# Performance work log

Hardware: AMD Instinct MI355X
Metric: run time of the kernel (lower is better)

## Reference

```python
import jax, jax.numpy as jnp
import numpy as np

B, S, D, H, BS, L, FF, V = 2, 4096, 1024, 16, 64, 4, 4096, 50000
HD = D // H; NB = S // BS; NM = NB - 2; R = 3

def layernorm(x, g, b):
    mu = x.mean(-1, keepdims=True)
    var = ((x - mu) ** 2).mean(-1, keepdims=True)
    return (x - mu) * jax.lax.rsqrt(var + 1e-5) * g + b

def bigbird_attn(x, neg, rand_attn, Wq, bq, Wk, bk, Wv, bv, Wo, bo):
    heads = lambda t: t.reshape(B, S, H, HD).transpose(0, 2, 1, 3)
    q, k, v = heads(x @ Wq + bq), heads(x @ Wk + bk), heads(x @ Wv + bv)
    scale = np.float32(1.0 / np.sqrt(HD))
    qb = q.reshape(B, H, NB, BS, HD); kb = k.reshape(B, H, NB, BS, HD); vb = v.reshape(B, H, NB, BS, HD)
    negb = neg.reshape(B, NB, BS)
    # global query blocks (first & last) attend densely to all keys
    qg = jnp.concatenate([qb[:, :, 0], qb[:, :, -1]], axis=2)  # [B,H,2*BS,HD]
    sg = jnp.einsum('bhqd,bhkd->bhqk', qg, k) * scale + neg[:, None, None, :]
    ctx_g = jnp.einsum('bhqk,bhkd->bhqd', jax.nn.softmax(sg, -1), v)
    # middle query blocks: sliding window(3) + global(2) + random(R) key blocks
    win_k = jnp.stack([kb[:, :, i:i + NM] for i in range(3)], axis=3)  # [B,H,NM,3,BS,HD]
    win_v = jnp.stack([vb[:, :, i:i + NM] for i in range(3)], axis=3)
    gidx = jnp.array([0, NB - 1])
    g_k = jnp.broadcast_to(kb[:, :, gidx][:, :, None], (B, H, NM, 2, BS, HD))
    g_v = jnp.broadcast_to(vb[:, :, gidx][:, :, None], (B, H, NM, 2, BS, HD))
    hix = jnp.arange(H)[:, None, None]
    r_k = kb[:, hix, rand_attn]  # [B,H,NM,R,BS,HD]
    r_v = vb[:, hix, rand_attn]
    K = 3 + 2 + R
    keys = jnp.concatenate([win_k, g_k, r_k], axis=3).reshape(B, H, NM, K * BS, HD)
    vals = jnp.concatenate([win_v, g_v, r_v], axis=3).reshape(B, H, NM, K * BS, HD)
    win_m = jnp.stack([negb[:, i:i + NM] for i in range(3)], axis=2)  # [B,NM,3,BS]
    g_m = jnp.broadcast_to(negb[:, gidx][:, None], (B, NM, 2, BS))
    m_wg = jnp.concatenate([win_m, g_m], axis=2).reshape(B, 1, NM, 5 * BS)
    r_m = negb[:, rand_attn].reshape(B, H, NM, R * BS)
    m_all = jnp.concatenate([jnp.broadcast_to(m_wg, (B, H, NM, 5 * BS)), r_m], axis=-1)
    sm = jnp.einsum('bhnqd,bhnkd->bhnqk', qb[:, :, 1:-1], keys) * scale + m_all[:, :, :, None, :]
    ctx_m = jnp.einsum('bhnqk,bhnkd->bhnqd', jax.nn.softmax(sm, -1), vals)
    ctx = jnp.concatenate([ctx_g[:, :, None, :BS], ctx_m, ctx_g[:, :, None, BS:]], axis=2)
    out = ctx.reshape(B, H, S, HD).transpose(0, 2, 1, 3).reshape(B, S, D)
    return out @ Wo + bo

def reference(input_ids, attention_mask, rand_attn, emb, Wq, bq, Wk, bk, Wv, bv, Wo, bo, ln1_g, ln1_b, W1, b1, W2, b2, ln2_g, ln2_b, lnf_g, lnf_b, projW, projb):
    x = emb[input_ids]
    neg = (1.0 - attention_mask.astype(jnp.float32)) * (-1e9)
    for l in range(L):  # pre-norm transformer encoder layers
        x = x + bigbird_attn(layernorm(x, ln1_g[l], ln1_b[l]), neg, rand_attn,
                             Wq[l], bq[l], Wk[l], bk[l], Wv[l], bv[l], Wo[l], bo[l])
        h = layernorm(x, ln2_g[l], ln2_b[l])
        x = x + (jax.nn.gelu(h @ W1[l] + b1[l]) @ W2[l] + b2[l])
    x = layernorm(x, lnf_g, lnf_b)
    feats = x.mean(axis=1)  # pooled output (mean over tokens)
    feats = feats / jnp.maximum(jnp.linalg.norm(feats, axis=-1, keepdims=True), 1e-12)
    return feats @ projW + projb

def setup_inputs():
    key = jax.random.key(0)
    ks = jax.random.split(key, 16)
    init = lambda k, shp: (0.02 * jax.random.normal(k, shp)).astype(jnp.float32)
    return {
        'input_ids': jax.random.randint(ks[0], (B, S), 0, V),
        'attention_mask': jnp.ones((B, S), dtype=jnp.int32),
        'rand_attn': jax.random.randint(ks[1], (H, NM, R), 1, NB - 1),
        'emb': init(ks[2], (V, D)),
        'Wq': init(ks[3], (L, D, D)), 'bq': jnp.zeros((L, D), jnp.float32),
        'Wk': init(ks[4], (L, D, D)), 'bk': jnp.zeros((L, D), jnp.float32),
        'Wv': init(ks[5], (L, D, D)), 'bv': jnp.zeros((L, D), jnp.float32),
        'Wo': init(ks[6], (L, D, D)), 'bo': jnp.zeros((L, D), jnp.float32),
        'ln1_g': jnp.ones((L, D), jnp.float32), 'ln1_b': jnp.zeros((L, D), jnp.float32),
        'W1': init(ks[7], (L, D, FF)), 'b1': jnp.zeros((L, FF), jnp.float32),
        'W2': init(ks[8], (L, FF, D)), 'b2': jnp.zeros((L, D), jnp.float32),
        'ln2_g': jnp.ones((L, D), jnp.float32), 'ln2_b': jnp.zeros((L, D), jnp.float32),
        'lnf_g': jnp.ones((D,), jnp.float32), 'lnf_b': jnp.zeros((D,), jnp.float32),
        'projW': init(ks[9], (D, 512)), 'projb': jnp.zeros((512,), jnp.float32),
    }
```

## Files before the change

kernel.cpp:

```cpp
#include <hip/hip_runtime.h>
#include <hip/hip_bf16.h>
#include <cstdint>
#include <cstddef>

#define BATCH 2
#define SEQ   4096
#define DIM   1024
#define NHEAD 16
#define HDIM  64
#define NBLK  64
#define NMID  62
#define NRAND 3
#define NLAYER 4
#define FFDIM 4096
#define ROWS  (BATCH*SEQ)
#define KSPL  8
#define QKVLD (3*DIM)
#define WLAYER (12*1024*1024)

using f32x4 = __attribute__((ext_vector_type(4))) float;
using s16x8 = __attribute__((ext_vector_type(8))) short;
using s16x4 = __attribute__((ext_vector_type(4))) short;

__device__ inline float bf2f(short s) {
    unsigned u = ((unsigned)(unsigned short)s) << 16;
    union { unsigned u; float f; } cv; cv.u = u; return cv.f;
}
__device__ inline short f2bf(float f) {
    union { float f; unsigned u; } cv; cv.f = f;
    unsigned u = cv.u;
    unsigned r = (u + 0x7fffu + ((u >> 16) & 1u)) >> 16;
    return (short)r;
}
__device__ inline float gelu_f(float x) {
    float u = 0.7978845608028654f * (x + 0.044715f * x * x * x);
    float a = fabsf(u);
    float th = 1.f - 2.f / (1.f + __expf(2.f * a));
    th = copysignf(th, u);
    return 0.5f * x * (1.f + th);
}

__device__ inline void gload16(const short* g, short* l) {
    __builtin_amdgcn_global_load_lds(
        (const __attribute__((address_space(1))) void*)g,
        (__attribute__((address_space(3))) void*)l,
        16, 0, 0);
}

__global__ __launch_bounds__(256) void embed_kernel(
    const int* __restrict__ ids, const float* __restrict__ emb, float* __restrict__ x)
{
    int row = blockIdx.x;
    int id  = ids[row];
    ((float4*)x)[(size_t)row * 256 + threadIdx.x] =
        ((const float4*)emb)[(size_t)id * 256 + threadIdx.x];
}

__global__ __launch_bounds__(256) void neg_kernel(
    const int* __restrict__ mask, float* __restrict__ neg)
{
    int i = blockIdx.x * 256 + threadIdx.x;
    if (i < ROWS) neg[i] = (1.f - (float)mask[i]) * -1e9f;
}

__global__ __launch_bounds__(256) void biaspack_kernel(
    const float* __restrict__ bq, const float* __restrict__ bk,
    const float* __restrict__ bv, float* __restrict__ b3)
{
    int i = blockIdx.x * 256 + threadIdx.x;
    float v = (i < DIM) ? bq[i] : (i < 2 * DIM) ? bk[i - DIM] : bv[i - 2 * DIM];
    b3[i] = v;
}

template<int OUTBF>
__global__ __launch_bounds__(256) void ln_kernel(
    const float* __restrict__ x, const float* __restrict__ g,
    const float* __restrict__ bia, void* __restrict__ out)
{
    __shared__ float s1[4], s2[4];
    int row = blockIdx.x, t = threadIdx.x;
    const float* xr = x + (size_t)row * DIM;
    float4 v = ((const float4*)xr)[t];
    float s = v.x + v.y + v.z + v.w;
    #pragma unroll
    for (int o = 32; o > 0; o >>= 1) s += __shfl_xor(s, o, 64);
    if ((t & 63) == 0) s1[t >> 6] = s;
    __syncthreads();
    float mu = (s1[0] + s1[1] + s1[2] + s1[3]) * (1.f / DIM);
    float dx = v.x - mu, dy = v.y - mu, dz = v.z - mu, dw = v.w - mu;
    float q = dx*dx + dy*dy + dz*dz + dw*dw;
    #pragma unroll
    for (int o = 32; o > 0; o >>= 1) q += __shfl_xor(q, o, 64);
    if ((t & 63) == 0) s2[t >> 6] = q;
    __syncthreads();
    float var = (s2[0] + s2[1] + s2[2] + s2[3]) * (1.f / DIM);
    float rs  = rsqrtf(var + 1e-5f);
    float4 gg = ((const float4*)g)[t];
    float4 bb = ((const float4*)bia)[t];
    float o0 = dx * rs * gg.x + bb.x;
    float o1 = dy * rs * gg.y + bb.y;
    float o2 = dz * rs * gg.z + bb.z;
    float o3 = dw * rs * gg.w + bb.w;
    if (OUTBF) {
        s16x4 ov = { f2bf(o0), f2bf(o1), f2bf(o2), f2bf(o3) };
        ((s16x4*)out)[(size_t)row * (DIM/4) + t] = ov;
    } else {
        float4 ov = { o0, o1, o2, o3 };
        ((float4*)out)[(size_t)row * (DIM/4) + t] = ov;
    }
}

__global__ __launch_bounds__(256) void wconv_kernel(
    const float* __restrict__ W, short* __restrict__ Wt, int K, int N)
{
    __shared__ float tile[32][33];
    int k0 = blockIdx.x * 32, n0 = blockIdx.y * 32;
    int t = threadIdx.x;
    int r = t >> 3, c = (t & 7) * 4;
    float4 v = *(const float4*)(W + (size_t)(k0 + r) * N + n0 + c);
    tile[r][c+0] = v.x; tile[r][c+1] = v.y; tile[r][c+2] = v.z; tile[r][c+3] = v.w;
    __syncthreads();
    s16x4 ov;
    #pragma unroll
    for (int jj = 0; jj < 4; ++jj) ov[jj] = f2bf(tile[c + jj][r]);
    *(s16x4*)(Wt + (size_t)(n0 + r) * K + k0 + c) = ov;
}

__global__ __launch_bounds__(256) void vtrans_kernel(
    const short* __restrict__ qkv, short* __restrict__ vT)
{
    __shared__ short tile[64][66];
    const int sb = blockIdx.x, h = blockIdx.y, b = blockIdx.z;
    const int t = threadIdx.x;
    {
        int row = t >> 2, c0 = (t & 3) * 16;
        const short* src = qkv + 2 * DIM + (size_t)(b * SEQ + sb * 64 + row) * QKVLD + h * HDIM + c0;
        s16x8 a0 = ((const s16x8*)src)[0];
        s16x8 a1 = ((const s16x8*)src)[1];
        #pragma unroll
        for (int i = 0; i < 8; ++i) { tile[row][c0 + i] = a0[i]; tile[row][c0 + 8 + i] = a1[i]; }
    }
    __syncthreads();
    {
        int d = t >> 2, k0 = (t & 3) * 16;
        s16x8 o0, o1;
        #pragma unroll
        for (int i = 0; i < 8; ++i) { o0[i] = tile[k0 + i][d]; o1[i] = tile[k0 + 8 + i][d]; }
        short* dst = vT + (size_t)((b * NHEAD + h) * HDIM + d) * SEQ + sb * 64 + k0;
        ((s16x8*)dst)[0] = o0;
        ((s16x8*)dst)[1] = o1;
    }
}

template<int EPI>
__global__ __launch_bounds__(512) void gemm256_kernel(
    const short* __restrict__ A, const short* __restrict__ Bt,
    const float* __restrict__ bias, const float* __restrict__ resid,
    void* __restrict__ Cout, int M, int N, int K, int klen)
{
    __shared__ short As[2][256 * 64];
    __shared__ short Bs[2][256 * 64];
    const int t = threadIdx.x;
    const int m0 = blockIdx.x * 256, n0 = blockIdx.y * 256;
    const int lane = t & 63, wave = t >> 6;
    const int wm = wave >> 2, wn = wave & 3;
    const int l15 = lane & 15;
    const int lrow = lane >> 3;
    const int lksw = ((lane & 7) ^ lrow) * 8;
    const int ga = wn;
    const int hb = wn >> 1, gb = wm * 2 + (wn & 1);

    f32x4 acc[8][4];
    #pragma unroll
    for (int m = 0; m < 8; ++m)
        #pragma unroll
        for (int n = 0; n < 4; ++n)
            acc[m][n] = f32x4{0.f, 0.f, 0.f, 0.f};

    auto STAGE_A = [&](int side, int kt) {
        #pragma unroll
        for (int c = 0; c < 4; ++c) {
            int row = wm * 128 + c * 32 + ga * 8 + lrow;
            gload16(A + (size_t)(m0 + row) * K + kt + lksw,
                    &As[side][wm * 8192 + c * 2048 + ga * 512]);
        }
    };
    auto STAGE_B = [&](int side, int kt) {
        #pragma unroll
        for (int c = 0; c < 4; ++c) {
            int row = hb * 128 + c * 32 + gb * 8 + lrow;
            gload16(Bt + (size_t)(n0 + row) * K + kt + lksw,
                    &Bs[side][hb * 8192 + c * 2048 + gb * 512]);
        }
    };
    auto RD_A = [&](const short* buf, int mf, int kk) -> s16x8 {
        int r = wm * 128 + mf * 16 + l15;
        int cb = kk * 64 + (lane >> 4) * 16;
        return *(const s16x8*)((const char*)buf + r * 128 + (cb ^ ((r & 7) << 4)));
    };
    auto RD_B = [&](const short* buf, int nf, int kk) -> s16x8 {
        int r = wn * 64 + nf * 16 + l15;
        int cb = kk * 64 + (lane >> 4) * 16;
        return *(const s16x8*)((const char*)buf + r * 128 + (cb ^ ((r & 7) << 4)));
    };

    const int k0 = blockIdx.z * klen, kend = k0 + klen;
    STAGE_A(0, k0);
    STAGE_B(0, k0);
    asm volatile("s_waitcnt vmcnt(0)" ::: "memory");
    __syncthreads();

    int cur = 0;
    for (int kt = k0; kt < kend; kt += 64) {
        const short* Ac = As[cur];
        const short* Bc = Bs[cur];
        const bool nxt = (kt + 64 < kend);
        s16x8 af[4][2], bf[2][2], bf2[2][2];

        #pragma unroll
        for (int mf = 0; mf < 4; ++mf) { af[mf][0] = RD_A(Ac, mf, 0); af[mf][1] = RD_A(Ac, mf, 1); }
        #pragma unroll
        for (int nf = 0; nf < 2; ++nf) { bf[nf][0] = RD_B(Bc, nf, 0); bf[nf][1] = RD_B(Bc, nf, 1); }
        if (nxt) STAGE_A(cur ^ 1, kt + 64);
        __builtin_amdgcn_s_barrier();
        __builtin_amdgcn_s_setprio(1);
        #pragma unroll
        for (int kk = 0; kk < 2; ++kk)
            #pragma unroll
            for (int mf = 0; mf < 4; ++mf)
                #pragma unroll
                for (int nf = 0; nf < 2; ++nf)
                    acc[mf][nf] = __builtin_amdgcn_mfma_f32_16x16x32_bf16(af[mf][kk], bf[nf][kk], acc[mf][nf], 0, 0, 0);
        __builtin_amdgcn_s_setprio(0);
        __builtin_amdgcn_s_barrier();

        #pragma unroll
        for (int nf = 0; nf < 2; ++nf) { bf2[nf][0] = RD_B(Bc, 2 + nf, 0); bf2[nf][1] = RD_B(Bc, 2 + nf, 1); }
        if (nxt) STAGE_B(cur ^ 1, kt + 64);
        __builtin_amdgcn_s_barrier();
        __builtin_amdgcn_s_setprio(1);
        #pragma unroll
        for (int kk = 0; kk < 2; ++kk)
            #pragma unroll
            for (int mf = 0; mf < 4; ++mf)
                #pragma unroll
                for (int nf = 0; nf < 2; ++nf)
                    acc[mf][2 + nf] = __builtin_amdgcn_mfma_f32_16x16x32_bf16(af[mf][kk], bf2[nf][kk], acc[mf][2 + nf], 0, 0, 0);
        __builtin_amdgcn_s_setprio(0);
        __builtin_amdgcn_s_barrier();

        #pragma unroll
        for (int mf = 0; mf < 4; ++mf) { af[mf][0] = RD_A(Ac, 4 + mf, 0); af[mf][1] = RD_A(Ac, 4 + mf, 1); }
        __builtin_amdgcn_s_barrier();
        __builtin_amdgcn_s_setprio(1);
        #pragma unroll
        for (int kk = 0; kk < 2; ++kk)
            #pragma unroll
            for (int mf = 0; mf < 4; ++mf)
                #pragma unroll
                for (int nf = 0; nf < 2; ++nf)
                    acc[4 + mf][nf] = __builtin_amdgcn_mfma_f32_16x16x32_bf16(af[mf][kk], bf[nf][kk], acc[4 + mf][nf], 0, 0, 0);
        __builtin_amdgcn_s_setprio(0);
        __builtin_amdgcn_s_barrier();

        asm volatile("s_waitcnt vmcnt(0)" ::: "memory");
        __builtin_amdgcn_s_barrier();
        __builtin_amdgcn_s_setprio(1);
        #pragma unroll
        for (int kk = 0; kk < 2; ++kk)
            #pragma unroll
            for (int mf = 0; mf < 4; ++mf)
                #pragma unroll
                for (int nf = 0; nf < 2; ++nf)
                    acc[4 + mf][2 + nf] = __builtin_amdgcn_mfma_f32_16x16x32_bf16(af[mf][kk], bf2[nf][kk], acc[4 + mf][2 + nf], 0, 0, 0);
        __builtin_amdgcn_s_setprio(0);
        __builtin_amdgcn_s_barrier();

        cur ^= 1;
    }

    const int rbase = m0 + wm * 128 + ((lane >> 4) << 2);
    const int cbase = n0 + wn * 64 + l15;
    #pragma unroll
    for (int m = 0; m < 8; ++m) {
        #pragma unroll
        for (int n = 0; n < 4; ++n) {
            #pragma unroll
            for (int j = 0; j < 4; ++j) {
                int row = rbase + m * 16 + j;
                int col = cbase + n * 16;
                size_t idx = (size_t)row * N + col;
                float val = acc[m][n][j];
                if (EPI == 3) {
                    ((float*)Cout)[(size_t)blockIdx.z * ((size_t)M * N) + idx] = val;
                } else {
                    val += bias[col];
                    if (EPI == 1) val = gelu_f(val);
                    ((short*)Cout)[idx] = f2bf(val);
                }
            }
        }
    }
    (void)resid;
}

template<int EPI>
__global__ __launch_bounds__(256) void gemm_kernel(
    const short* __restrict__ A, const short* __restrict__ Bt,
    const float* __restrict__ bias, const float* __restrict__ resid,
    void* __restrict__ Cout, int M, int N, int K, int klen)
{
    __shared__ short As[128 * 64];
    __shared__ short Bs[128 * 64];
    const int t = threadIdx.x;
    const int m0 = blockIdx.x * 128, n0 = blockIdx.y * 128;
    const int lane = t & 63, wave = t >> 6;
    const int wr = (wave >> 1) * 64, wc = (wave & 1) * 64;
    const int lrow = lane >> 3;
    const int lksw = ((lane & 7) ^ lrow) * 8;

    f32x4 acc[4][4];
    #pragma unroll
    for (int m = 0; m < 4; ++m)
        #pragma unroll
        for (int n = 0; n < 4; ++n)
            acc[m][n] = f32x4{0.f, 0.f, 0.f, 0.f};

    const int k0 = blockIdx.z * klen;
    for (int kt = k0; kt < k0 + klen; kt += 64) {
        #pragma unroll
        for (int c = 0; c < 4; ++c) {
            int chunk = wave * 4 + c;
            int row = chunk * 8 + lrow;
            gload16(A  + (size_t)(m0 + row) * K + kt + lksw, As + chunk * 512);
            gload16(Bt + (size_t)(n0 + row) * K + kt + lksw, Bs + chunk * 512);
        }
        asm volatile("s_waitcnt vmcnt(0)" ::: "memory");
        __syncthreads();
        #pragma unroll
        for (int kk = 0; kk < 2; ++kk) {
            s16x8 af[4], bfr[4];
            int cb = kk * 64 + (lane >> 4) * 16;
            #pragma unroll
            for (int i = 0; i < 4; ++i) {
                int rA = wr + i * 16 + (lane & 15);
                af[i]  = *(const s16x8*)((const char*)As + rA * 128 + (cb ^ ((rA & 7) << 4)));
                int rB = wc + i * 16 + (lane & 15);
                bfr[i] = *(const s16x8*)((const char*)Bs + rB * 128 + (cb ^ ((rB & 7) << 4)));
            }
            #pragma unroll
            for (int m = 0; m < 4; ++m)
                #pragma unroll
                for (int n = 0; n < 4; ++n)
                    acc[m][n] = __builtin_amdgcn_mfma_f32_16x16x32_bf16(
                        af[m], bfr[n], acc[m][n], 0, 0, 0);
        }
        __syncthreads();
    }

    const int rbase = m0 + wr + ((lane >> 4) << 2);
    const int cbase = n0 + wc + (lane & 15);
    #pragma unroll
    for (int m = 0; m < 4; ++m) {
        #pragma unroll
        for (int n = 0; n < 4; ++n) {
            #pragma unroll
            for (int j = 0; j < 4; ++j) {
                int row = rbase + m * 16 + j;
                int col = cbase + n * 16;
                size_t idx = (size_t)row * N + col;
                float val = acc[m][n][j] + bias[col];
                if (EPI == 1) val = gelu_f(val);
                if (EPI == 2) ((float*)Cout)[idx] = val + resid[idx];
                else          ((short*)Cout)[idx] = f2bf(val);
            }
        }
    }
}

__global__ __launch_bounds__(256) void kred_kernel(
    const float* __restrict__ part, const float* __restrict__ bias, float* __restrict__ x)
{
    const size_t MN = (size_t)ROWS * DIM;
    size_t idx = (size_t)blockIdx.x * DIM + threadIdx.x * 4;
    float4 p0 = *(const float4*)(part + idx);
    float4 p1 = *(const float4*)(part + MN + idx);
    float4 bb = *(const float4*)(bias + threadIdx.x * 4);
    float4 xv = *(const float4*)(x + idx);
    float4 o = { xv.x + p0.x + p1.x + bb.x,
                 xv.y + p0.y + p1.y + bb.y,
                 xv.z + p0.z + p1.z + bb.z,
                 xv.w + p0.w + p1.w + bb.w };
    *(float4*)(x + idx) = o;
}

__device__ inline void attn_tile_mfma(
    const short* __restrict__ kglob, const short* __restrict__ vtglob,
    const float* __restrict__ negp, int kld,
    short* Ks, short* Vs, float* kmask,
    const s16x8* qfrag, f32x4* o, float& mr, float& lsum)
{
    const int t = threadIdx.x;
    const int lane = t & 63;
    const int q15 = lane & 15, g = lane >> 4;
    const int sw = (lane & 7) << 4;

    {
        int row = t >> 2, c0 = (t & 3) * 16;
        int rsw = (row & 7) << 4;
        const short* ksrc = kglob + (size_t)row * kld + c0;
        s16x8 a0 = ((const s16x8*)ksrc)[0];
        s16x8 a1 = ((const s16x8*)ksrc)[1];
        char* kdst = (char*)Ks + row * 128;
        *(s16x8*)(kdst + ((c0 * 2)      ^ rsw)) = a0;
        *(s16x8*)(kdst + ((c0 * 2 + 16) ^ rsw)) = a1;
        const short* vsrc = vtglob + (size_t)row * SEQ + c0;
        s16x8 b0 = ((const s16x8*)vsrc)[0];
        s16x8 b1 = ((const s16x8*)vsrc)[1];
        char* vdst = (char*)Vs + row * 128;
        *(s16x8*)(vdst + ((c0 * 2)      ^ rsw)) = b0;
        *(s16x8*)(vdst + ((c0 * 2 + 16) ^ rsw)) = b1;
        if (t < 16) ((float4*)kmask)[t] = ((const float4*)negp)[t];
    }
    __syncthreads();

    f32x4 s[4];
    #pragma unroll
    for (int f = 0; f < 4; ++f) s[f] = f32x4{0.f, 0.f, 0.f, 0.f};
    #pragma unroll
    for (int ch = 0; ch < 2; ++ch) {
        #pragma unroll
        for (int f = 0; f < 4; ++f) {
            s16x8 kf = *(const s16x8*)((const char*)Ks + (16 * f + q15) * 128 + ((ch * 64 + g * 16) ^ sw));
            s[f] = __builtin_amdgcn_mfma_f32_16x16x32_bf16(kf, qfrag[ch], s[f], 0, 0, 0);
        }
    }

    float p[4][4];
    float mt = -1e30f;
    #pragma unroll
    for (int f = 0; f < 4; ++f) {
        float4 km = ((const float4*)kmask)[f * 4 + g];
        #pragma unroll
        for (int j = 0; j < 4; ++j) {
            float val = s[f][j] * 0.125f + ((const float*)&km)[j];
            p[f][j] = val;
            mt = fmaxf(mt, val);
        }
    }
    mt = fmaxf(mt, __shfl_xor(mt, 16, 64));
    mt = fmaxf(mt, __shfl_xor(mt, 32, 64));
    float mn = fmaxf(mr, mt);
    float psum = 0.f;
    #pragma unroll
    for (int f = 0; f < 4; ++f)
        #pragma unroll
        for (int j = 0; j < 4; ++j) {
            float e = __expf(p[f][j] - mn);
            p[f][j] = e;
            psum += e;
        }
    psum += __shfl_xor(psum, 16, 64);
    psum += __shfl_xor(psum, 32, 64);
    float fc = __expf(mr - mn);
    mr = mn;
    lsum = lsum * fc + psum;
    #pragma unroll
    for (int dt = 0; dt < 4; ++dt)
        #pragma unroll
        for (int j = 0; j < 4; ++j) o[dt][j] *= fc;

    unsigned pk[4][2];
    #pragma unroll
    for (int f = 0; f < 4; ++f)
        #pragma unroll
        for (int pp = 0; pp < 2; ++pp)
            pk[f][pp] = ((unsigned)(unsigned short)f2bf(p[f][2 * pp + 1]) << 16)
                      |  (unsigned)(unsigned short)f2bf(p[f][2 * pp]);

    const int bsel = (lane >> 4) & 1, asel = (lane >> 5) & 1;
    #pragma unroll
    for (int c = 0; c < 2; ++c) {
        union { s16x8 v; int u[4]; } pb;
        #pragma unroll
        for (int w = 0; w < 4; ++w) {
            int src = q15 + 16 * (2 * bsel + (w >> 1));
            int lo = __shfl((int)pk[2 * c][w & 1], src, 64);
            int hi = __shfl((int)pk[2 * c + 1][w & 1], src, 64);
            pb.u[w] = asel ? hi : lo;
        }
        #pragma unroll
        for (int dt = 0; dt < 4; ++dt) {
            s16x8 vf = *(const s16x8*)((const char*)Vs + (16 * dt + q15) * 128 + ((c * 64 + g * 16) ^ sw));
            o[dt] = __builtin_amdgcn_mfma_f32_16x16x32_bf16(vf, pb.v, o[dt], 0, 0, 0);
        }
    }
    __syncthreads();
}

__device__ inline void stage_q64_swz(const short* __restrict__ qglob, int qld, short* Qs)
{
    int t = threadIdx.x;
    int row = t >> 2, c0 = (t & 3) * 16;
    int rsw = (row & 7) << 4;
    const short* src = qglob + (size_t)row * qld + c0;
    s16x8 a0 = ((const s16x8*)src)[0];
    s16x8 a1 = ((const s16x8*)src)[1];
    char* dst = (char*)Qs + row * 128;
    *(s16x8*)(dst + ((c0 * 2)      ^ rsw)) = a0;
    *(s16x8*)(dst + ((c0 * 2 + 16) ^ rsw)) = a1;
}

__global__ __launch_bounds__(256) void attn_middle_mfma(
    const short* __restrict__ qkv, const short* __restrict__ vT,
    const float* __restrict__ neg, const int* __restrict__ rand_attn, short* __restrict__ ctx)
{
    __shared__ short Qs[64 * 64];
    __shared__ short Ks[64 * 64];
    __shared__ short Vs[64 * 64];
    __shared__ float kmask[64];

    const int j = blockIdx.x, h = blockIdx.y, b = blockIdx.z;
    const int n = j + 1;
    const int t = threadIdx.x;
    const int lane = t & 63, wave = t >> 6;
    const int q15 = lane & 15, g = lane >> 4;
    const int sw = (lane & 7) << 4;

    stage_q64_swz(qkv + (size_t)(b * SEQ + n * 64) * QKVLD + h * HDIM, QKVLD, Qs);
    __syncthreads();

    s16x8 qfrag[2];
    {
        int qrow = wave * 16 + q15;
        #pragma unroll
        for (int ch = 0; ch < 2; ++ch)
            qfrag[ch] = *(const s16x8*)((const char*)Qs + qrow * 128 + ((ch * 64 + g * 16) ^ sw));
    }

    int kbl[8];
    kbl[0] = n - 1; kbl[1] = n; kbl[2] = n + 1; kbl[3] = 0; kbl[4] = NBLK - 1;
    {
        const int* ra = rand_attn + ((size_t)h * NMID + j) * NRAND;
        kbl[5] = ra[0]; kbl[6] = ra[1]; kbl[7] = ra[2];
    }

    f32x4 o[4];
    #pragma unroll
    for (int dt = 0; dt < 4; ++dt) o[dt] = f32x4{0.f, 0.f, 0.f, 0.f};
    float mr = -1e30f, lsum = 0.f;

    const short* kbase  = qkv + DIM + (size_t)b * SEQ * QKVLD + h * HDIM;
    const short* vtbase = vT + (size_t)(b * NHEAD + h) * HDIM * SEQ;
    const float* negb   = neg + (size_t)b * SEQ;

    #pragma unroll 1
    for (int ib = 0; ib < 8; ++ib) {
        int kbn = kbl[ib];
        attn_tile_mfma(kbase + (size_t)kbn * 64 * QKVLD, vtbase + kbn * 64,
                       negb + kbn * 64, QKVLD, Ks, Vs, kmask, qfrag, o, mr, lsum);
    }

    float inv = 1.f / lsum;
    short* obase = ctx + (size_t)(b * SEQ + n * 64 + wave * 16 + q15) * DIM + h * HDIM;
    #pragma unroll
    for (int dt = 0; dt < 4; ++dt) {
        s16x4 ov;
        #pragma unroll
        for (int jj = 0; jj < 4; ++jj) ov[jj] = f2bf(o[dt][jj] * inv);
        *(s16x4*)(obase + dt * 16 + g * 4) = ov;
    }
}

__global__ __launch_bounds__(256) void attn_global_mfma(
    const short* __restrict__ qkv, const short* __restrict__ vT,
    const float* __restrict__ neg, float* __restrict__ part)
{
    __shared__ short Qs[64 * 64];
    __shared__ short Ks[64 * 64];
    __shared__ short Vs[64 * 64];
    __shared__ float kmask[64];

    const int qb = blockIdx.x >> 3, ks = blockIdx.x & 7;
    const int h = blockIdx.y, b = blockIdx.z;
    const int tok0 = qb ? (SEQ - 64) : 0;
    const int t = threadIdx.x;
    const int lane = t & 63, wave = t >> 6;
    const int q15 = lane & 15, g = lane >> 4;
    const int sw = (lane & 7) << 4;

    stage_q64_swz(qkv + (size_t)(b * SEQ + tok0) * QKVLD + h * HDIM, QKVLD, Qs);
    __syncthreads();

    s16x8 qfrag[2];
    {
        int qrow = wave * 16 + q15;
        #pragma unroll
        for (int ch = 0; ch < 2; ++ch)
            qfrag[ch] = *(const s16x8*)((const char*)Qs + qrow * 128 + ((ch * 64 + g * 16) ^ sw));
    }

    f32x4 o[4];
    #pragma unroll
    for (int dt = 0; dt < 4; ++dt) o[dt] = f32x4{0.f, 0.f, 0.f, 0.f};
    float mr = -1e30f, lsum = 0.f;

    const short* kbase  = qkv + DIM + (size_t)b * SEQ * QKVLD + h * HDIM;
    const short* vtbase = vT + (size_t)(b * NHEAD + h) * HDIM * SEQ;
    const float* negb   = neg + (size_t)b * SEQ;

    #pragma unroll 1
    for (int ib = 0; ib < 8; ++ib) {
        int kbn = ks * 8 + ib;
        attn_tile_mfma(kbase + (size_t)kbn * 64 * QKVLD, vtbase + kbn * 64,
                       negb + kbn * 64, QKVLD, Ks, Vs, kmask, qfrag, o, mr, lsum);
    }

    float* pbase = part + ((size_t)(((b * NHEAD + h) * 2 + qb) * KSPL + ks)) * 4224;
    int qrow = wave * 16 + q15;
    #pragma unroll
    for (int dt = 0; dt < 4; ++dt)
        *(f32x4*)(pbase + qrow * 64 + dt * 16 + g * 4) = o[dt];
    if (g == 0) { pbase[4096 + qrow] = mr; pbase[4160 + qrow] = lsum; }
}

__global__ __launch_bounds__(256) void attn_greduce(
    const float* __restrict__ part, short* __restrict__ ctx)
{
    const int qb = blockIdx.x, h = blockIdx.y, b = blockIdx.z;
    const int tok0 = qb ? (SEQ - 64) : 0;
    const int t = threadIdx.x;
    const int qq = t >> 2, d0 = (t & 3) * 16;
    const float* base = part + ((size_t)(((b * NHEAD + h) * 2 + qb) * KSPL)) * 4224;

    float m = -1e30f;
    #pragma unroll 1
    for (int s = 0; s < KSPL; ++s)
        m = fmaxf(m, base[(size_t)s * 4224 + 4096 + qq]);
    float L = 0.f;
    float acc[16];
    #pragma unroll
    for (int i = 0; i < 16; ++i) acc[i] = 0.f;
    #pragma unroll 1
    for (int s = 0; s < KSPL; ++s) {
        const float* bp = base + (size_t)s * 4224;
        float w = __expf(bp[4096 + qq] - m);
        L += w * bp[4160 + qq];
        const float4* row = (const float4*)(bp + qq * 64 + d0);
        #pragma unroll
        for (int v4 = 0; v4 < 4; ++v4) {
            float4 val = row[v4];
            acc[v4 * 4 + 0] = fmaf(w, val.x, acc[v4 * 4 + 0]);
            acc[v4 * 4 + 1] = fmaf(w, val.y, acc[v4 * 4 + 1]);
            acc[v4 * 4 + 2] = fmaf(w, val.z, acc[v4 * 4 + 2]);
            acc[v4 * 4 + 3] = fmaf(w, val.w, acc[v4 * 4 + 3]);
        }
    }
    float inv = 1.f / L;
    short* dst = ctx + (size_t)(b * SEQ + tok0 + qq) * DIM + h * HDIM + d0;
    s16x8 o0, o1;
    #pragma unroll
    for (int i = 0; i < 8; ++i) { o0[i] = f2bf(acc[i] * inv); o1[i] = f2bf(acc[8 + i] * inv); }
    ((s16x8*)dst)[0] = o0;
    ((s16x8*)dst)[1] = o1;
}

__global__ __launch_bounds__(256) void colsum1_kernel(
    const float* __restrict__ xln, float* __restrict__ partial)
{
    const int ch = blockIdx.x, b = blockIdx.y, t = threadIdx.x;
    const float* base = xln + ((size_t)b * SEQ + ch * 32) * DIM + t * 4;
    float4 acc = {0.f, 0.f, 0.f, 0.f};
    #pragma unroll 4
    for (int r = 0; r < 32; ++r) {
        float4 v = *(const float4*)(base + (size_t)r * DIM);
        acc.x += v.x; acc.y += v.y; acc.z += v.z; acc.w += v.w;
    }
    *(float4*)(partial + ((size_t)(b * 128 + ch)) * DIM + t * 4) = acc;
}

__global__ __launch_bounds__(256) void colsum2_kernel(
    const float* __restrict__ partial, float* __restrict__ feats)
{
    const int b = blockIdx.x, t = threadIdx.x;
    float4 acc = {0.f, 0.f, 0.f, 0.f};
    #pragma unroll 1
    for (int ch = 0; ch < 128; ++ch) {
        float4 v = *(const float4*)(partial + ((size_t)(b * 128 + ch)) * DIM + t * 4);
        acc.x += v.x; acc.y += v.y; acc.z += v.z; acc.w += v.w;
    }
    const float is = 1.f / SEQ;
    float4 o = { acc.x * is, acc.y * is, acc.z * is, acc.w * is };
    *(float4*)(feats + (size_t)b * DIM + t * 4) = o;
}

__global__ __launch_bounds__(256) void head_kernel(
    const float* __restrict__ feats, const float* __restrict__ projW,
    const float* __restrict__ projb, float* __restrict__ out)
{
    __shared__ float f[DIM];
    __shared__ float slots[4];
    int b = blockIdx.x, t = threadIdx.x;
    float ss = 0.f;
    for (int i = t; i < DIM; i += 256) {
        float vv = feats[b * DIM + i];
        f[i] = vv;
        ss += vv * vv;
    }
    #pragma unroll
    for (int o = 32; o > 0; o >>= 1) ss += __shfl_xor(ss, o, 64);
    if ((t & 63) == 0) slots[t >> 6] = ss;
    __syncthreads();
    float nrm = sqrtf(slots[0] + slots[1] + slots[2] + slots[3]);
    float inv = 1.f / fmaxf(nrm, 1e-12f);
    for (int o = t; o < 512; o += 256) {
        float acc = 0.f;
        for (int d = 0; d < DIM; ++d)
            acc = fmaf(f[d], projW[(size_t)d * 512 + o], acc);
        out[b * 512 + o] = acc * inv + projb[o];
    }
}

extern "C" void kernel_launch(void* const* d_in, const int* in_sizes, int n_in,
                              void* d_out, int out_size, void* d_ws, size_t ws_size,
                              hipStream_t stream)
{
    (void)in_sizes; (void)n_in; (void)out_size; (void)ws_size;
    const int*   ids   = (const int*)d_in[0];
    const int*   amask = (const int*)d_in[1];
    const int*   rnd   = (const int*)d_in[2];
    const float* emb   = (const float*)d_in[3];
    const float* Wq    = (const float*)d_in[4];
    const float* bq    = (const float*)d_in[5];
    const float* Wk    = (const float*)d_in[6];
    const float* bk    = (const float*)d_in[7];
    const float* Wv    = (const float*)d_in[8];
    const float* bv    = (const float*)d_in[9];
    const float* Wo    = (const float*)d_in[10];
    const float* bo    = (const float*)d_in[11];
    const float* ln1g  = (const float*)d_in[12];
    const float* ln1b  = (const float*)d_in[13];
    const float* W1    = (const float*)d_in[14];
    const float* b1    = (const float*)d_in[15];
    const float* W2    = (const float*)d_in[16];
    const float* b2    = (const float*)d_in[17];
    const float* ln2g  = (const float*)d_in[18];
    const float* ln2b  = (const float*)d_in[19];
    const float* lnfg  = (const float*)d_in[20];
    const float* lnfb  = (const float*)d_in[21];
    const float* projW = (const float*)d_in[22];
    const float* projb = (const float*)d_in[23];
    float* out = (float*)d_out;

    char* ws = (char*)d_ws;
    size_t off = 0;
    float* x    = (float*)(ws + off); off += (size_t)ROWS * DIM * 4;
    float* xn_f = (float*)(ws + off);
    short* xn_b = (short*)(ws + off); off += (size_t)ROWS * DIM * 4;
    short* qkv  = (short*)(ws + off); off += (size_t)ROWS * QKVLD * 2;
    short* vT   = (short*)(ws + off); off += (size_t)ROWS * DIM * 2;
    short* ctxb = (short*)(ws + off); off += (size_t)ROWS * DIM * 2;
    short* ffb  = (short*)(ws + off); off += (size_t)ROWS * FFDIM * 2;
    short* wt4  = (short*)(ws + off); off += (size_t)NLAYER * WLAYER * 2;
    float* neg  = (float*)(ws + off); off += (size_t)ROWS * 4;
    float* bias3= (float*)(ws + off); off += (size_t)NLAYER * QKVLD * 4;
    float* feats= (float*)(ws + off); off += (size_t)BATCH * DIM * 4;
    float* part = (float*)(ws + off); off += (size_t)BATCH * NHEAD * 2 * KSPL * 4224 * 4;
    float* cpart= (float*)(ws + off); off += (size_t)BATCH * 128 * DIM * 4;
    float* ff2p = (float*)qkv;

    embed_kernel<<<ROWS, 256, 0, stream>>>(ids, emb, x);
    neg_kernel<<<(ROWS + 255) / 256, 256, 0, stream>>>(amask, neg);

    for (int l = 0; l < NLAYER; ++l) {
        short* wq3 = wt4 + (size_t)l * WLAYER;
        short* wo  = wq3 + 3 * 1024 * 1024;
        short* w1t = wo  + 1024 * 1024;
        short* w2t = w1t + 4 * 1024 * 1024;
        wconv_kernel<<<dim3(DIM/32, DIM/32), 256, 0, stream>>>(Wq + (size_t)l*DIM*DIM, wq3,               DIM, DIM);
        wconv_kernel<<<dim3(DIM/32, DIM/32), 256, 0, stream>>>(Wk + (size_t)l*DIM*DIM, wq3 + 1024*1024,   DIM, DIM);
        wconv_kernel<<<dim3(DIM/32, DIM/32), 256, 0, stream>>>(Wv + (size_t)l*DIM*DIM, wq3 + 2*1024*1024, DIM, DIM);
        wconv_kernel<<<dim3(DIM/32, DIM/32), 256, 0, stream>>>(Wo + (size_t)l*DIM*DIM, wo, DIM, DIM);
        wconv_kernel<<<dim3(DIM/32, FFDIM/32), 256, 0, stream>>>(W1 + (size_t)l*DIM*FFDIM, w1t, DIM, FFDIM);
        wconv_kernel<<<dim3(FFDIM/32, DIM/32), 256, 0, stream>>>(W2 + (size_t)l*FFDIM*DIM, w2t, FFDIM, DIM);
        biaspack_kernel<<<QKVLD/256, 256, 0, stream>>>(bq + l*DIM, bk + l*DIM, bv + l*DIM, bias3 + (size_t)l*QKVLD);
    }

    for (int l = 0; l < NLAYER; ++l) {
        short* wq3 = wt4 + (size_t)l * WLAYER;
        short* wo  = wq3 + 3 * 1024 * 1024;
        short* w1t = wo  + 1024 * 1024;
        short* w2t = w1t + 4 * 1024 * 1024;

        ln_kernel<1><<<ROWS, 256, 0, stream>>>(x, ln1g + l * DIM, ln1b + l * DIM, xn_b);

        gemm256_kernel<0><<<dim3(ROWS/256, QKVLD/256), 512, 0, stream>>>(xn_b, wq3, bias3 + (size_t)l*QKVLD, nullptr, qkv, ROWS, QKVLD, DIM, DIM);

        vtrans_kernel<<<dim3(SEQ/64, NHEAD, BATCH), 256, 0, stream>>>(qkv, vT);

        attn_global_mfma<<<dim3(2 * KSPL, NHEAD, BATCH), 256, 0, stream>>>(qkv, vT, neg, part);
        attn_middle_mfma<<<dim3(NMID, NHEAD, BATCH), 256, 0, stream>>>(qkv, vT, neg, rnd, ctxb);
        attn_greduce<<<dim3(2, NHEAD, BATCH), 256, 0, stream>>>(part, ctxb);

        gemm_kernel<2><<<dim3(ROWS/128, DIM/128), 256, 0, stream>>>(ctxb, wo, bo + l*DIM, x, x, ROWS, DIM, DIM, DIM);

        ln_kernel<1><<<ROWS, 256, 0, stream>>>(x, ln2g + l * DIM, ln2b + l * DIM, xn_b);

        gemm256_kernel<1><<<dim3(ROWS/256, FFDIM/256), 512, 0, stream>>>(xn_b, w1t, b1 + l*FFDIM, nullptr, ffb, ROWS, FFDIM, DIM, DIM);
        gemm256_kernel<3><<<dim3(ROWS/256, DIM/256, 2), 512, 0, stream>>>(ffb, w2t, nullptr, nullptr, ff2p, ROWS, DIM, FFDIM, FFDIM/2);
        kred_kernel<<<ROWS, 256, 0, stream>>>(ff2p, b2 + l*DIM, x);
    }

    ln_kernel<0><<<ROWS, 256, 0, stream>>>(x, lnfg, lnfb, xn_f);
    colsum1_kernel<<<dim3(SEQ/32, BATCH), 256, 0, stream>>>(xn_f, cpart);
    colsum2_kernel<<<BATCH, 256, 0, stream>>>(cpart, feats);
    head_kernel<<<BATCH, 256, 0, stream>>>(feats, projW, projb, out);
}
```

Before: 1.792 ms.

## Batch weight conversions, fuse split-K reduce with next LayerNorm, swizzle GEMM tiles

Merges the per-layer weight transpose/convert and bias pack launches into a few batched launches indexed by blockIdx.z or y. Fuses the FFN split-K reduction and residual add with the following LayerNorm (next layer's ln1 or the final LN), which removes one full pass over x per layer. Also remaps the workgroup id in the 256-tile GEMM to group tiles for better L2 locality. In the last layer, x is not written back, which relies on nothing reading x afterwards.

```diff
diff --git a/kernel.cpp b/kernel.cpp
--- a/kernel.cpp
+++ b/kernel.cpp
@@ -68,8 +68,11 @@
     const float* __restrict__ bv, float* __restrict__ b3)
 {
     int i = blockIdx.x * 256 + threadIdx.x;
-    float v = (i < DIM) ? bq[i] : (i < 2 * DIM) ? bk[i - DIM] : bv[i - 2 * DIM];
-    b3[i] = v;
+    int l = blockIdx.y;
+    float v = (i < DIM) ? bq[l * DIM + i]
+            : (i < 2 * DIM) ? bk[l * DIM + i - DIM]
+            : bv[l * DIM + i - 2 * DIM];
+    b3[(size_t)l * QKVLD + i] = v;
 }
 
 template<int OUTBF>
@@ -110,8 +113,8 @@
     }
 }
 
-__global__ __launch_bounds__(256) void wconv_kernel(
-    const float* __restrict__ W, short* __restrict__ Wt, int K, int N)
+__device__ inline void wconv_body(const float* __restrict__ W, short* __restrict__ Wt,
+                                  int K, int N)
 {
     __shared__ float tile[32][33];
     int k0 = blockIdx.x * 32, n0 = blockIdx.y * 32;
@@ -124,6 +127,25 @@
     #pragma unroll
     for (int jj = 0; jj < 4; ++jj) ov[jj] = f2bf(tile[c + jj][r]);
     *(s16x4*)(Wt + (size_t)(n0 + r) * K + k0 + c) = ov;
+}
+
+__global__ __launch_bounds__(256) void wconv4_kernel(
+    const float* __restrict__ Wq, const float* __restrict__ Wk,
+    const float* __restrict__ Wv, const float* __restrict__ Wo,
+    short* __restrict__ wt4)
+{
+    int z = blockIdx.z, l = z >> 2, m = z & 3;
+    const float* W = (m == 0 ? Wq : m == 1 ? Wk : m == 2 ? Wv : Wo) + (size_t)l * DIM * DIM;
+    short* Wt = wt4 + (size_t)l * WLAYER + (size_t)m * 1024 * 1024;
+    wconv_body(W, Wt, DIM, DIM);
+}
+
+__global__ __launch_bounds__(256) void wconvff_kernel(
+    const float* __restrict__ W, short* __restrict__ wt4,
+    int K, int N, size_t dstOff)
+{
+    int l = blockIdx.z;
+    wconv_body(W + (size_t)l * DIM * FFDIM, wt4 + (size_t)l * WLAYER + dstOff, K, N);
 }
 
 __global__ __launch_bounds__(256) void vtrans_kernel(
@@ -155,13 +177,17 @@
 template<int EPI>
 __global__ __launch_bounds__(512) void gemm256_kernel(
     const short* __restrict__ A, const short* __restrict__ Bt,
-    const float* __restrict__ bias, const float* __restrict__ resid,
-    void* __restrict__ Cout, int M, int N, int K, int klen)
+    const float* __restrict__ bias, void* __restrict__ Cout,
+    int M, int N, int K, int klen)
 {
     __shared__ short As[2][256 * 64];
     __shared__ short Bs[2][256 * 64];
     const int t = threadIdx.x;
-    const int m0 = blockIdx.x * 256, n0 = blockIdx.y * 256;
+    const int nwg = gridDim.x * gridDim.y;
+    const int id  = blockIdx.y * gridDim.x + blockIdx.x;
+    const int cpx = nwg >> 3;
+    const int swz = (id & 7) * cpx + (id >> 3);
+    const int m0 = (swz % gridDim.x) * 256, n0 = (swz / gridDim.x) * 256;
     const int lane = t & 63, wave = t >> 6;
     const int wm = wave >> 2, wn = wave & 3;
     const int l15 = lane & 15;
@@ -301,7 +327,6 @@
             }
         }
     }
-    (void)resid;
 }
 
 template<int EPI>
@@ -378,20 +403,53 @@
     }
 }
 
-__global__ __launch_bounds__(256) void kred_kernel(
-    const float* __restrict__ part, const float* __restrict__ bias, float* __restrict__ x)
-{
+template<int MODE>
+__global__ __launch_bounds__(256) void kred_ln_kernel(
+    const float* __restrict__ part, const float* __restrict__ bias,
+    const float* __restrict__ g, const float* __restrict__ bvec,
+    float* __restrict__ x, void* __restrict__ xn)
+{
+    __shared__ float s1[4], s2[4];
     const size_t MN = (size_t)ROWS * DIM;
-    size_t idx = (size_t)blockIdx.x * DIM + threadIdx.x * 4;
+    const int row = blockIdx.x, t = threadIdx.x;
+    size_t idx = (size_t)row * DIM + t * 4;
     float4 p0 = *(const float4*)(part + idx);
     float4 p1 = *(const float4*)(part + MN + idx);
-    float4 bb = *(const float4*)(bias + threadIdx.x * 4);
+    float4 bb = *(const float4*)(bias + t * 4);
     float4 xv = *(const float4*)(x + idx);
-    float4 o = { xv.x + p0.x + p1.x + bb.x,
+    float4 v = { xv.x + p0.x + p1.x + bb.x,
                  xv.y + p0.y + p1.y + bb.y,
                  xv.z + p0.z + p1.z + bb.z,
                  xv.w + p0.w + p1.w + bb.w };
-    *(float4*)(x + idx) = o;
+    if (MODE == 0) *(float4*)(x + idx) = v;
+
+    float s = v.x + v.y + v.z + v.w;
+    #pragma unroll
+    for (int o = 32; o > 0; o >>= 1) s += __shfl_xor(s, o, 64);
+    if ((t & 63) == 0) s1[t >> 6] = s;
+    __syncthreads();
+    float mu = (s1[0] + s1[1] + s1[2] + s1[3]) * (1.f / DIM);
+    float dx = v.x - mu, dy = v.y - mu, dz = v.z - mu, dw = v.w - mu;
+    float q = dx*dx + dy*dy + dz*dz + dw*dw;
+    #pragma unroll
+    for (int o = 32; o > 0; o >>= 1) q += __shfl_xor(q, o, 64);
+    if ((t & 63) == 0) s2[t >> 6] = q;
+    __syncthreads();
+    float var = (s2[0] + s2[1] + s2[2] + s2[3]) * (1.f / DIM);
+    float rs  = rsqrtf(var + 1e-5f);
+    float4 gg = ((const float4*)g)[t];
+    float4 b2 = ((const float4*)bvec)[t];
+    float o0 = dx * rs * gg.x + b2.x;
+    float o1 = dy * rs * gg.y + b2.y;
+    float o2 = dz * rs * gg.z + b2.z;
+    float o3 = dw * rs * gg.w + b2.w;
+    if (MODE == 0) {
+        s16x4 ov = { f2bf(o0), f2bf(o1), f2bf(o2), f2bf(o3) };
+        ((s16x4*)xn)[(size_t)row * (DIM/4) + t] = ov;
+    } else {
+        float4 ov = { o0, o1, o2, o3 };
+        ((float4*)xn)[(size_t)row * (DIM/4) + t] = ov;
+    }
 }
 
 __device__ inline void attn_tile_mfma(
@@ -772,29 +830,21 @@
     embed_kernel<<<ROWS, 256, 0, stream>>>(ids, emb, x);
     neg_kernel<<<(ROWS + 255) / 256, 256, 0, stream>>>(amask, neg);
 
+    wconv4_kernel<<<dim3(DIM/32, DIM/32, NLAYER*4), 256, 0, stream>>>(Wq, Wk, Wv, Wo, wt4);
+    wconvff_kernel<<<dim3(DIM/32, FFDIM/32, NLAYER), 256, 0, stream>>>(W1, wt4, DIM, FFDIM, (size_t)4*1024*1024);
+    wconvff_kernel<<<dim3(FFDIM/32, DIM/32, NLAYER), 256, 0, stream>>>(W2, wt4, FFDIM, DIM, (size_t)8*1024*1024);
+    biaspack_kernel<<<dim3(QKVLD/256, NLAYER), 256, 0, stream>>>(bq, bk, bv, bias3);
+
     for (int l = 0; l < NLAYER; ++l) {
         short* wq3 = wt4 + (size_t)l * WLAYER;
         short* wo  = wq3 + 3 * 1024 * 1024;
         short* w1t = wo  + 1024 * 1024;
         short* w2t = w1t + 4 * 1024 * 1024;
-        wconv_kernel<<<dim3(DIM/32, DIM/32), 256, 0, stream>>>(Wq + (size_t)l*DIM*DIM, wq3,               DIM, DIM);
-        wconv_kernel<<<dim3(DIM/32, DIM/32), 256, 0, stream>>>(Wk + (size_t)l*DIM*DIM, wq3 + 1024*1024,   DIM, DIM);
-        wconv_kernel<<<dim3(DIM/32, DIM/32), 256, 0, stream>>>(Wv + (size_t)l*DIM*DIM, wq3 + 2*1024*1024, DIM, DIM);
-        wconv_kernel<<<dim3(DIM/32, DIM/32), 256, 0, stream>>>(Wo + (size_t)l*DIM*DIM, wo, DIM, DIM);
-        wconv_kernel<<<dim3(DIM/32, FFDIM/32), 256, 0, stream>>>(W1 + (size_t)l*DIM*FFDIM, w1t, DIM, FFDIM);
-        wconv_kernel<<<dim3(FFDIM/32, DIM/32), 256, 0, stream>>>(W2 + (size_t)l*FFDIM*DIM, w2t, FFDIM, DIM);
-        biaspack_kernel<<<QKVLD/256, 256, 0, stream>>>(bq + l*DIM, bk + l*DIM, bv + l*DIM, bias3 + (size_t)l*QKVLD);
-    }
-
-    for (int l = 0; l < NLAYER; ++l) {
-        short* wq3 = wt4 + (size_t)l * WLAYER;
-        short* wo  = wq3 + 3 * 1024 * 1024;
-        short* w1t = wo  + 1024 * 1024;
-        short* w2t = w1t + 4 * 1024 * 1024;
-
-        ln_kernel<1><<<ROWS, 256, 0, stream>>>(x, ln1g + l * DIM, ln1b + l * DIM, xn_b);
-
-        gemm256_kernel<0><<<dim3(ROWS/256, QKVLD/256), 512, 0, stream>>>(xn_b, wq3, bias3 + (size_t)l*QKVLD, nullptr, qkv, ROWS, QKVLD, DIM, DIM);
+
+        if (l == 0)
+            ln_kernel<1><<<ROWS, 256, 0, stream>>>(x, ln1g, ln1b, xn_b);
+
+        gemm256_kernel<0><<<dim3(ROWS/256, QKVLD/256), 512, 0, stream>>>(xn_b, wq3, bias3 + (size_t)l*QKVLD, qkv, ROWS, QKVLD, DIM, DIM);
 
         vtrans_kernel<<<dim3(SEQ/64, NHEAD, BATCH), 256, 0, stream>>>(qkv, vT);
 
@@ -806,12 +856,15 @@
 
         ln_kernel<1><<<ROWS, 256, 0, stream>>>(x, ln2g + l * DIM, ln2b + l * DIM, xn_b);
 
-        gemm256_kernel<1><<<dim3(ROWS/256, FFDIM/256), 512, 0, stream>>>(xn_b, w1t, b1 + l*FFDIM, nullptr, ffb, ROWS, FFDIM, DIM, DIM);
-        gemm256_kernel<3><<<dim3(ROWS/256, DIM/256, 2), 512, 0, stream>>>(ffb, w2t, nullptr, nullptr, ff2p, ROWS, DIM, FFDIM, FFDIM/2);
-        kred_kernel<<<ROWS, 256, 0, stream>>>(ff2p, b2 + l*DIM, x);
-    }
-
-    ln_kernel<0><<<ROWS, 256, 0, stream>>>(x, lnfg, lnfb, xn_f);
+        gemm256_kernel<1><<<dim3(ROWS/256, FFDIM/256), 512, 0, stream>>>(xn_b, w1t, b1 + l*FFDIM, ffb, ROWS, FFDIM, DIM, DIM);
+        gemm256_kernel<3><<<dim3(ROWS/256, DIM/256, 2), 512, 0, stream>>>(ffb, w2t, nullptr, ff2p, ROWS, DIM, FFDIM, FFDIM/2);
+
+        if (l < NLAYER - 1)
+            kred_ln_kernel<0><<<ROWS, 256, 0, stream>>>(ff2p, b2 + l*DIM, ln1g + (l+1)*DIM, ln1b + (l+1)*DIM, x, xn_b);
+        else
+            kred_ln_kernel<1><<<ROWS, 256, 0, stream>>>(ff2p, b2 + l*DIM, lnfg, lnfb, x, xn_f);
+    }
+
     colsum1_kernel<<<dim3(SEQ/32, BATCH), 256, 0, stream>>>(xn_f, cpart);
     colsum2_kernel<<<BATCH, 256, 0, stream>>>(cpart, feats);
     head_kernel<<<BATCH, 256, 0, stream>>>(feats, projW, projb, out);
```

Measured after the change: 1.825 ms. No clear change (+1.9%).
